# Kernel tuning notes

Hardware: AMD Instinct MI355X
Metric: run time of the kernel (lower is better)

Reference implementation:

```python
import jax, jax.numpy as jnp
import numpy as np

BETA = 0.5
ITEM_NUM = 100000
REGION_NUM = 1000
EMBED = 128
HIDDEN = 256
B, H = 1024, 256


def setup_inputs() -> dict:
    key = jax.random.key(0)
    ks = jax.random.split(key, 10)
    history = jax.random.randint(ks[0], (B, H), 0, ITEM_NUM)
    target = jax.random.randint(ks[1], (B,), 0, ITEM_NUM)
    history_region = jax.random.randint(ks[2], (B, H), 0, REGION_NUM)
    target_region = jax.random.randint(ks[3], (B,), 0, REGION_NUM)
    E_hist = 0.01 * jax.random.normal(ks[4], (ITEM_NUM, EMBED), dtype=jnp.float32)
    E_targ = 0.01 * jax.random.normal(ks[5], (ITEM_NUM, EMBED), dtype=jnp.float32)
    E_reg = 0.01 * jax.random.normal(ks[6], (REGION_NUM, EMBED), dtype=jnp.float32)
    lim1 = 1.0 / np.sqrt(2 * EMBED)
    W1 = jax.random.uniform(ks[7], (2 * EMBED, HIDDEN), jnp.float32, -lim1, lim1)
    b1 = jnp.zeros((HIDDEN,), jnp.float32)
    lim2 = 1.0 / np.sqrt(HIDDEN)
    w2 = jax.random.uniform(ks[8], (HIDDEN,), jnp.float32, -lim2, lim2)
    return {"history": history, "target": target,
            "history_region": history_region, "target_region": target_region,
            "E_hist": E_hist, "E_targ": E_targ, "E_reg": E_reg,
            "W1": W1, "b1": b1, "w2": w2}


def reference(history, target, history_region, target_region,
              E_hist, E_targ, E_reg, W1, b1, w2):
    # gathers + concat: hist [B,H,2d], tgt [B,2d]
    hist = jnp.concatenate([E_hist[history], E_reg[history_region]], axis=-1)
    tgt = jnp.concatenate([E_targ[target], E_reg[target_region]], axis=-1)
    # elementwise product broadcast over history dim
    inp = hist * tgt[:, None, :]                      # [B,H,2d]
    hid = jax.nn.relu(jnp.einsum('bhd,dk->bhk', inp, W1) + b1)
    scores = jnp.einsum('bhk,k->bh', hid, w2)         # [B,H]
    mask = (history != target[:, None]).astype(scores.dtype)
    exp_a = jnp.exp(scores) * mask                    # [B,H]
    denom = jnp.power(jnp.sum(exp_a, axis=-1), BETA)  # [B]
    attn = exp_a / denom[:, None]                     # [B,H]
    # weighted reduction: sum_h sum_d hist*attn*tgt
    pred = jnp.einsum('bhd,bh,bd->b', hist, attn, tgt)
    return jax.nn.sigmoid(pred)
```

## Files before the change

kernel.cpp:

```cpp
#include <hip/hip_runtime.h>
#include <hip/hip_bf16.h>

#define NB 1024
#define NH 256
#define EMB 128
#define TWOD 256
#define HID 256
#define ROWS 128
#define BPB 2
#define NBLK (NB * BPB)

typedef __attribute__((ext_vector_type(4))) float f32x4;
typedef __attribute__((ext_vector_type(8))) short bf16x8;

__device__ __forceinline__ unsigned short f2bf(float f) {
  union { float f; unsigned u; } v; v.f = f;
  unsigned u = v.u;
  unsigned r = (u + 0x7fffu + ((u >> 16) & 1u)) >> 16;
  return (unsigned short)r;
}

__global__ __launch_bounds__(256) void prep_w1t(const float* __restrict__ W1,
                                                unsigned short* __restrict__ W1T) {
  const int d = blockIdx.x;
  const int n = threadIdx.x;
  W1T[(size_t)n * TWOD + d] = f2bf(W1[(size_t)d * HID + n]);
}

__global__ __launch_bounds__(512, 4) void nais_main(
    const int* __restrict__ history, const int* __restrict__ target,
    const int* __restrict__ hregion, const int* __restrict__ tregion,
    const float* __restrict__ E_hist, const float* __restrict__ E_targ,
    const float* __restrict__ E_reg,
    const unsigned short* __restrict__ W1T, const float* __restrict__ b1,
    const float* __restrict__ w2,
    float* __restrict__ part_se, float* __restrict__ part_sd)
{
  const int blk = blockIdx.x;
  const int b = blk >> 1;
  const int r0 = (blk & 1) * ROWS;
  const int tid = threadIdx.x;
  const int lane = tid & 63;
  const int wave = tid >> 6;
  const int l15 = lane & 15;
  const int lhi = lane >> 4;
  const int l31 = lane & 31;
  const int halfsel = lane >> 5;

  __shared__ __align__(16) unsigned short inp_lds[ROWS * 256];
  __shared__ float dot_lds[ROWS];
  __shared__ int items_lds[ROWS];
  __shared__ float score_parts[8][ROWS];

  const float* tsrc = halfsel ? (E_reg + (size_t)tregion[b] * EMB)
                              : (E_targ + (size_t)target[b] * EMB);
  const f32x4 t = *(const f32x4*)(tsrc + l31 * 4);
  const int tgt_item = target[b];

  const int* keysrc = halfsel ? hregion : history;
  const float* table = halfsel ? E_reg : E_hist;

  {
    int key[16];
    #pragma unroll
    for (int s = 0; s < 16; ++s)
      key[s] = keysrc[b * NH + r0 + wave * 16 + s];

    f32x4 vb[16];
    #pragma unroll
    for (int s = 0; s < 16; ++s)
      vb[s] = *(const f32x4*)(table + (size_t)key[s] * EMB + l31 * 4);

    #pragma unroll
    for (int s = 0; s < 16; ++s) {
      const int row = wave * 16 + s;
      if (lane == 0) items_lds[row] = key[s];
      f32x4 v = vb[s] * t;
      float ds = v[0] + v[1] + v[2] + v[3];
      ds += __shfl_xor(ds, 1);
      ds += __shfl_xor(ds, 2);
      ds += __shfl_xor(ds, 4);
      ds += __shfl_xor(ds, 8);
      ds += __shfl_xor(ds, 16);
      ds += __shfl_xor(ds, 32);
      if (lane == 0) dot_lds[row] = ds;

      float2 f01; f01.x = v[0]; f01.y = v[1];
      float2 f23; f23.x = v[2]; f23.y = v[3];
      __hip_bfloat162 p0 = __float22bfloat162_rn(f01);
      __hip_bfloat162 p1 = __float22bfloat162_rn(f23);
      union { __hip_bfloat162 h; unsigned u; } c0, c1;
      c0.h = p0; c1.h = p1;
      const int g = halfsel * 16 + (l31 >> 1);
      const int gs = g ^ (row & 7) ^ ((g >> 3) & 3);
      unsigned* dst = (unsigned*)&inp_lds[row * 256 + gs * 8 + (lane & 1) * 4];
      dst[0] = c0.u; dst[1] = c1.u;
    }
  }
  __syncthreads();

  {
    const int col0 = wave * 32;
    float b1v[2], w2v[2];
    #pragma unroll
    for (int n = 0; n < 2; ++n) {
      const int colh = col0 + n * 16 + l15;
      b1v[n] = b1[colh];
      w2v[n] = w2[colh];
    }

    f32x4 acc[2][4][2];
    #pragma unroll
    for (int c = 0; c < 2; ++c)
      #pragma unroll
      for (int m = 0; m < 4; ++m)
        #pragma unroll
        for (int n = 0; n < 2; ++n)
          acc[c][m][n] = (f32x4){0.f, 0.f, 0.f, 0.f};

    #pragma unroll
    for (int kk = 0; kk < 8; ++kk) {
      bf16x8 bfr[2];
      #pragma unroll
      for (int n = 0; n < 2; ++n) {
        const int colh = col0 + n * 16 + l15;
        bfr[n] = *(const bf16x8*)(W1T + (size_t)colh * TWOD + kk * 32 + lhi * 8);
      }
      bf16x8 af[2][4];
      #pragma unroll
      for (int c = 0; c < 2; ++c)
        #pragma unroll
        for (int m = 0; m < 4; ++m) {
          const int row = c * 64 + m * 16 + l15;
          const int gk = kk * 4 + lhi;
          const int gs = gk ^ (row & 7) ^ ((gk >> 3) & 3);
          af[c][m] = *(const bf16x8*)(&inp_lds[row * 256 + gs * 8]);
        }
      __builtin_amdgcn_s_setprio(1);
      #pragma unroll
      for (int c = 0; c < 2; ++c)
        #pragma unroll
        for (int m = 0; m < 4; ++m)
          #pragma unroll
          for (int n = 0; n < 2; ++n)
            acc[c][m][n] = __builtin_amdgcn_mfma_f32_16x16x32_bf16(af[c][m], bfr[n], acc[c][m][n], 0, 0, 0);
      __builtin_amdgcn_s_setprio(0);
    }

    #pragma unroll
    for (int c = 0; c < 2; ++c) {
      #pragma unroll
      for (int m = 0; m < 4; ++m) {
        #pragma unroll
        for (int r = 0; r < 4; ++r) {
          float p = 0.f;
          #pragma unroll
          for (int n = 0; n < 2; ++n) {
            float hv = acc[c][m][n][r] + b1v[n];
            hv = hv > 0.f ? hv : 0.f;
            p += hv * w2v[n];
          }
          p += __shfl_xor(p, 1);
          p += __shfl_xor(p, 2);
          p += __shfl_xor(p, 4);
          p += __shfl_xor(p, 8);
          if (l15 == 0) score_parts[wave][c * 64 + m * 16 + lhi * 4 + r] = p;
        }
      }
    }
  }
  __syncthreads();

  if (wave < 2) {
    const int lrow = wave * 64 + lane;
    float sc = 0.f;
    #pragma unroll
    for (int w = 0; w < 8; ++w) sc += score_parts[w][lrow];
    float e = (items_lds[lrow] != tgt_item) ? expf(sc) : 0.f;
    float ed = e * dot_lds[lrow];
    #pragma unroll
    for (int off = 32; off >= 1; off >>= 1) {
      e += __shfl_xor(e, off);
      ed += __shfl_xor(ed, off);
    }
    if (lane == 0) {
      part_se[blk * 2 + wave] = e;
      part_sd[blk * 2 + wave] = ed;
    }
  }
}

__global__ __launch_bounds__(256) void finalize(const float* __restrict__ part_se,
                                                const float* __restrict__ part_sd,
                                                float* __restrict__ out) {
  const int b = blockIdx.x * 256 + threadIdx.x;
  if (b < NB) {
    float se = 0.f, sd = 0.f;
    #pragma unroll
    for (int i = 0; i < BPB * 2; ++i) {
      se += part_se[b * BPB * 2 + i];
      sd += part_sd[b * BPB * 2 + i];
    }
    const float pred = (se > 0.f) ? (sd / sqrtf(se)) : 0.f;
    out[b] = 1.f / (1.f + expf(-pred));
  }
}

extern "C" void kernel_launch(void* const* d_in, const int* in_sizes, int n_in,
                              void* d_out, int out_size, void* d_ws, size_t ws_size,
                              hipStream_t stream) {
  const int* history = (const int*)d_in[0];
  const int* target  = (const int*)d_in[1];
  const int* hregion = (const int*)d_in[2];
  const int* tregion = (const int*)d_in[3];
  const float* E_hist = (const float*)d_in[4];
  const float* E_targ = (const float*)d_in[5];
  const float* E_reg  = (const float*)d_in[6];
  const float* W1 = (const float*)d_in[7];
  const float* b1 = (const float*)d_in[8];
  const float* w2 = (const float*)d_in[9];
  float* out = (float*)d_out;

  unsigned short* W1T = (unsigned short*)d_ws;
  char* p = (char*)d_ws + (size_t)TWOD * HID * sizeof(unsigned short);
  float* part_se = (float*)p;        p += (size_t)NBLK * 2 * sizeof(float);
  float* part_sd = (float*)p;

  prep_w1t<<<TWOD, HID, 0, stream>>>(W1, W1T);
  nais_main<<<NBLK, 512, 0, stream>>>(history, target, hregion, tregion,
                                      E_hist, E_targ, E_reg, W1T, b1, w2,
                                      part_se, part_sd);
  finalize<<<(NB + 255) / 256, 256, 0, stream>>>(part_se, part_sd, out);
}
```

Measured before the change: 89.49 us.

## Pre-convert embedding tables to bf16 and gather rows directly into LDS

Adds a prep kernel that converts the full history and region embedding tables to bf16 each call. The main kernel then gathers bf16 rows straight into LDS with global_load_lds and applies the target product and dot sum in place before the MFMA stage. This halves gather bytes and LDS footprint, but adds a full-table conversion pass over the 100k-row table on every launch and computes the dot term from bf16-rounded history values.

```diff
diff --git a/kernel.cpp b/kernel.cpp
--- a/kernel.cpp
+++ b/kernel.cpp
@@ -9,6 +9,8 @@
 #define ROWS 128
 #define BPB 2
 #define NBLK (NB * BPB)
+#define HISTN 100000
+#define REGN 1000
 
 typedef __attribute__((ext_vector_type(4))) float f32x4;
 typedef __attribute__((ext_vector_type(8))) short bf16x8;
@@ -20,6 +22,23 @@
   return (unsigned short)r;
 }
 
+__device__ __forceinline__ float bf2f(short s) {
+  union { unsigned u; float f; } c;
+  c.u = ((unsigned)(unsigned short)s) << 16;
+  return c.f;
+}
+
+__device__ __forceinline__ bf16x8 pack8(f32x4 a, f32x4 b) {
+  union { bf16x8 w; unsigned u[4]; } r;
+  float2 p;
+  union { __hip_bfloat162 h; unsigned u; } c;
+  p.x = a[0]; p.y = a[1]; c.h = __float22bfloat162_rn(p); r.u[0] = c.u;
+  p.x = a[2]; p.y = a[3]; c.h = __float22bfloat162_rn(p); r.u[1] = c.u;
+  p.x = b[0]; p.y = b[1]; c.h = __float22bfloat162_rn(p); r.u[2] = c.u;
+  p.x = b[2]; p.y = b[3]; c.h = __float22bfloat162_rn(p); r.u[3] = c.u;
+  return r.w;
+}
+
 __global__ __launch_bounds__(256) void prep_w1t(const float* __restrict__ W1,
                                                 unsigned short* __restrict__ W1T) {
   const int d = blockIdx.x;
@@ -27,11 +46,27 @@
   W1T[(size_t)n * TWOD + d] = f2bf(W1[(size_t)d * HID + n]);
 }
 
+__global__ __launch_bounds__(256) void prep_ebf(const float* __restrict__ Eh,
+                                                const float* __restrict__ Er,
+                                                unsigned short* __restrict__ EBH,
+                                                unsigned short* __restrict__ EBR) {
+  const long long NE_H = (long long)HISTN * EMB;
+  const long long NE_R = (long long)REGN * EMB;
+  long long i = ((long long)blockIdx.x * 256 + threadIdx.x) * 8;
+  if (i >= NE_H + NE_R) return;
+  const float* src; unsigned short* dst; long long off;
+  if (i < NE_H) { src = Eh; dst = EBH; off = i; }
+  else          { src = Er; dst = EBR; off = i - NE_H; }
+  f32x4 v0 = *(const f32x4*)(src + off);
+  f32x4 v1 = *(const f32x4*)(src + off + 4);
+  *(bf16x8*)(dst + off) = pack8(v0, v1);
+}
+
 __global__ __launch_bounds__(512, 4) void nais_main(
     const int* __restrict__ history, const int* __restrict__ target,
     const int* __restrict__ hregion, const int* __restrict__ tregion,
-    const float* __restrict__ E_hist, const float* __restrict__ E_targ,
-    const float* __restrict__ E_reg,
+    const float* __restrict__ E_targ, const float* __restrict__ E_reg,
+    const unsigned short* __restrict__ EBH, const unsigned short* __restrict__ EBR,
     const unsigned short* __restrict__ W1T, const float* __restrict__ b1,
     const float* __restrict__ w2,
     float* __restrict__ part_se, float* __restrict__ part_sd)
@@ -44,58 +79,75 @@
   const int wave = tid >> 6;
   const int l15 = lane & 15;
   const int lhi = lane >> 4;
-  const int l31 = lane & 31;
-  const int halfsel = lane >> 5;
-
-  __shared__ __align__(16) unsigned short inp_lds[ROWS * 256];
+
+  __shared__ __align__(16) unsigned short A_h[ROWS * EMB];
+  __shared__ __align__(16) unsigned short A_r[ROWS * EMB];
+  __shared__ __align__(16) float tgt_lds[TWOD];
+  __shared__ int keys_h[ROWS];
+  __shared__ int keys_r[ROWS];
   __shared__ float dot_lds[ROWS];
-  __shared__ int items_lds[ROWS];
   __shared__ float score_parts[8][ROWS];
 
-  const float* tsrc = halfsel ? (E_reg + (size_t)tregion[b] * EMB)
-                              : (E_targ + (size_t)target[b] * EMB);
-  const f32x4 t = *(const f32x4*)(tsrc + l31 * 4);
   const int tgt_item = target[b];
 
-  const int* keysrc = halfsel ? hregion : history;
-  const float* table = halfsel ? E_reg : E_hist;
-
-  {
-    int key[16];
-    #pragma unroll
-    for (int s = 0; s < 16; ++s)
-      key[s] = keysrc[b * NH + r0 + wave * 16 + s];
-
-    f32x4 vb[16];
-    #pragma unroll
-    for (int s = 0; s < 16; ++s)
-      vb[s] = *(const f32x4*)(table + (size_t)key[s] * EMB + l31 * 4);
-
-    #pragma unroll
-    for (int s = 0; s < 16; ++s) {
-      const int row = wave * 16 + s;
-      if (lane == 0) items_lds[row] = key[s];
-      f32x4 v = vb[s] * t;
-      float ds = v[0] + v[1] + v[2] + v[3];
-      ds += __shfl_xor(ds, 1);
-      ds += __shfl_xor(ds, 2);
-      ds += __shfl_xor(ds, 4);
-      ds += __shfl_xor(ds, 8);
-      ds += __shfl_xor(ds, 16);
-      ds += __shfl_xor(ds, 32);
-      if (lane == 0) dot_lds[row] = ds;
-
-      float2 f01; f01.x = v[0]; f01.y = v[1];
-      float2 f23; f23.x = v[2]; f23.y = v[3];
-      __hip_bfloat162 p0 = __float22bfloat162_rn(f01);
-      __hip_bfloat162 p1 = __float22bfloat162_rn(f23);
-      union { __hip_bfloat162 h; unsigned u; } c0, c1;
-      c0.h = p0; c1.h = p1;
-      const int g = halfsel * 16 + (l31 >> 1);
-      const int gs = g ^ (row & 7) ^ ((g >> 3) & 3);
-      unsigned* dst = (unsigned*)&inp_lds[row * 256 + gs * 8 + (lane & 1) * 4];
-      dst[0] = c0.u; dst[1] = c1.u;
-    }
+  if (tid < ROWS) {
+    keys_h[tid] = history[b * NH + r0 + tid];
+  } else if (tid < 2 * ROWS) {
+    keys_r[tid - ROWS] = hregion[b * NH + r0 + (tid - ROWS)];
+  } else {
+    const int c = tid - 2 * ROWS;
+    tgt_lds[c] = (c < EMB) ? E_targ[(size_t)target[b] * EMB + c]
+                           : E_reg[(size_t)tregion[b] * EMB + (c - EMB)];
+  }
+  __syncthreads();
+
+  {
+    #pragma unroll
+    for (int q = 0; q < 4; ++q) {
+      const int quad = wave * 4 + q;
+      const int r = quad * 4 + (lane >> 4);
+      const int g = (lane & 15) ^ (r & 7);
+      const int kh = keys_h[r];
+      const unsigned short* gh = EBH + (size_t)kh * EMB + g * 8;
+      __builtin_amdgcn_global_load_lds(
+          (const __attribute__((address_space(1))) void*)gh,
+          (__attribute__((address_space(3))) void*)&A_h[quad * 4 * EMB],
+          16, 0, 0);
+      const int kr = keys_r[r];
+      const unsigned short* gr = EBR + (size_t)kr * EMB + g * 8;
+      __builtin_amdgcn_global_load_lds(
+          (const __attribute__((address_space(1))) void*)gr,
+          (__attribute__((address_space(3))) void*)&A_r[quad * 4 * EMB],
+          16, 0, 0);
+    }
+  }
+  asm volatile("s_waitcnt vmcnt(0)" ::: "memory");
+  __syncthreads();
+
+  {
+    const int row = wave * 16 + (lane >> 2);
+    const int seg = lane & 3;
+    unsigned short* panel = (seg < 2) ? A_h : A_r;
+    const int g0 = (seg & 1) * 8;
+    float dsum = 0.f;
+    #pragma unroll
+    for (int j = 0; j < 8; ++j) {
+      const int g = (g0 + j) ^ (row & 7);
+      bf16x8* ap = (bf16x8*)&panel[row * EMB + g * 8];
+      bf16x8 a = *ap;
+      const int kg = seg * 64 + j * 8;
+      f32x4 t0 = *(const f32x4*)&tgt_lds[kg];
+      f32x4 t1 = *(const f32x4*)&tgt_lds[kg + 4];
+      f32x4 lo, hi;
+      #pragma unroll
+      for (int e = 0; e < 4; ++e) { lo[e] = bf2f(a[e]); hi[e] = bf2f(a[4 + e]); }
+      lo *= t0; hi *= t1;
+      dsum += lo[0] + lo[1] + lo[2] + lo[3] + hi[0] + hi[1] + hi[2] + hi[3];
+      *ap = pack8(lo, hi);
+    }
+    dsum += __shfl_xor(dsum, 1);
+    dsum += __shfl_xor(dsum, 2);
+    if (seg == 0) dot_lds[row] = dsum;
   }
   __syncthreads();
 
@@ -120,6 +172,7 @@
 
     #pragma unroll
     for (int kk = 0; kk < 8; ++kk) {
+      const unsigned short* panel = (kk < 4) ? A_h : A_r;
       bf16x8 bfr[2];
       #pragma unroll
       for (int n = 0; n < 2; ++n) {
@@ -132,9 +185,8 @@
         #pragma unroll
         for (int m = 0; m < 4; ++m) {
           const int row = c * 64 + m * 16 + l15;
-          const int gk = kk * 4 + lhi;
-          const int gs = gk ^ (row & 7) ^ ((gk >> 3) & 3);
-          af[c][m] = *(const bf16x8*)(&inp_lds[row * 256 + gs * 8]);
+          const int gk = ((kk & 3) * 4 + lhi) ^ (row & 7);
+          af[c][m] = *(const bf16x8*)&panel[row * EMB + gk * 8];
         }
       __builtin_amdgcn_s_setprio(1);
       #pragma unroll
@@ -176,7 +228,7 @@
     float sc = 0.f;
     #pragma unroll
     for (int w = 0; w < 8; ++w) sc += score_parts[w][lrow];
-    float e = (items_lds[lrow] != tgt_item) ? expf(sc) : 0.f;
+    float e = (keys_h[lrow] != tgt_item) ? expf(sc) : 0.f;
     float ed = e * dot_lds[lrow];
     #pragma unroll
     for (int off = 32; off >= 1; off >>= 1) {
@@ -221,14 +273,21 @@
   const float* w2 = (const float*)d_in[9];
   float* out = (float*)d_out;
 
-  unsigned short* W1T = (unsigned short*)d_ws;
-  char* p = (char*)d_ws + (size_t)TWOD * HID * sizeof(unsigned short);
-  float* part_se = (float*)p;        p += (size_t)NBLK * 2 * sizeof(float);
-  float* part_sd = (float*)p;
+  char* p = (char*)d_ws;
+  unsigned short* W1T = (unsigned short*)p;  p += (size_t)TWOD * HID * 2;
+  unsigned short* EBR = (unsigned short*)p;  p += (size_t)REGN * EMB * 2;
+  float* part_se = (float*)p;                p += (size_t)NBLK * 2 * 4;
+  float* part_sd = (float*)p;                p += (size_t)NBLK * 2 * 4;
+  unsigned short* EBH = (unsigned short*)p;
 
   prep_w1t<<<TWOD, HID, 0, stream>>>(W1, W1T);
+  {
+    const long long tot8 = ((long long)HISTN * EMB + (long long)REGN * EMB) / 8;
+    const int blocks = (int)((tot8 + 255) / 256);
+    prep_ebf<<<blocks, 256, 0, stream>>>(E_hist, E_reg, EBH, EBR);
+  }
   nais_main<<<NBLK, 512, 0, stream>>>(history, target, hregion, tregion,
-                                      E_hist, E_targ, E_reg, W1T, b1, w2,
+                                      E_targ, E_reg, EBH, EBR, W1T, b1, w2,
                                       part_se, part_sd);
   finalize<<<(NB + 255) / 256, 256, 0, stream>>>(part_se, part_sd, out);
 }
```

New measurement: 94.50 us. 5.6% more time.
